# Kernel tuning notes

Hardware: AMD Instinct MI355X
Metric: run time of the kernel (lower is better)

The kernel has to match this reference:

```python
import jax, jax.numpy as jnp
import numpy as np

B, S, HID = 1, 2048, 2048
NH, NKV, HD = 16, 4, 128
G = NH // NKV  # queries per kv head (repeat_interleave factor)
QPA = 128      # query_pre_attn_scalar
EPS = 1e-6
SCALE = QPA ** -0.5
NEG = -1e9


def rms_norm(x, w, eps=EPS):
    return x * jax.lax.rsqrt(jnp.mean(x * x, axis=-1, keepdims=True) + eps) * w


def rope(x, cos, sin):
    # x: [B,S,H,D]; cos/sin: [S,D/2].
    # torch apply_rotary_emb: complex (x[:d/2] + i*x[d/2:]) * (cos + i*sin),
    # real parts -> first half, imag parts -> second half.
    d2 = x.shape[-1] // 2
    x1, x2 = x[..., :d2], x[..., d2:]
    c = cos[None, :, None, :]
    s = sin[None, :, None, :]
    return jnp.concatenate([x1 * c - x2 * s, x1 * s + x2 * c], axis=-1)


def setup_inputs() -> dict:
    key = jax.random.key(0)
    ks = jax.random.split(key, 4)
    hidden_states = jax.random.normal(ks[0], (B, S, HID), jnp.float32)
    inv_freq = 1.0 / (10000.0 ** (jnp.arange(0, HD, 2, dtype=jnp.float32) / HD))
    ang = jnp.arange(S, dtype=jnp.float32)[:, None] * inv_freq[None, :]  # [S, D/2]
    cos, sin = jnp.cos(ang), jnp.sin(ang)
    kv_write_indices = jnp.arange(S, dtype=jnp.int32)
    k_cache = jnp.zeros((B, S, NKV, HD), jnp.float32)
    v_cache = jnp.zeros((B, S, NKV, HD), jnp.float32)
    causal = jnp.tril(jnp.ones((S, S), dtype=bool))
    mask = jnp.where(causal, 0.0, NEG).astype(jnp.float32)[None, None]  # [1,1,S,S]
    qkv_out = (NH + 2 * NKV) * HD
    wqkv = jax.random.normal(ks[1], (qkv_out, HID), jnp.float32) * 0.02
    bqkv = jnp.zeros((qkv_out,), jnp.float32)
    wo = jax.random.normal(ks[2], (HID, NH * HD), jnp.float32) * 0.02
    bo = jnp.zeros((HID,), jnp.float32)
    q_norm_w = jnp.ones((HD,), jnp.float32)
    k_norm_w = jnp.ones((HD,), jnp.float32)
    return {"hidden_states": hidden_states, "cos": cos, "sin": sin,
            "k_cache": k_cache, "v_cache": v_cache, "mask": mask,
            "wqkv": wqkv, "bqkv": bqkv, "wo": wo, "bo": bo,
            "q_norm_w": q_norm_w, "k_norm_w": k_norm_w,
            "kv_write_indices": kv_write_indices}


def reference(hidden_states, cos, sin, k_cache, v_cache, mask,
              wqkv, bqkv, wo, bo, q_norm_w, k_norm_w, kv_write_indices):
    qkv = hidden_states @ wqkv.T + bqkv  # [B,S,(NH+2*NKV)*HD]
    q_sz, kv_sz = NH * HD, NKV * HD
    xq = qkv[..., :q_sz].reshape(B, S, NH, HD)
    xk = qkv[..., q_sz:q_sz + kv_sz].reshape(B, S, NKV, HD)
    xv = qkv[..., q_sz + kv_sz:].reshape(B, S, NKV, HD)
    xq = rope(rms_norm(xq, q_norm_w), cos, sin)
    xk = rope(rms_norm(xk, k_norm_w), cos, sin)
    k = k_cache.at[:, kv_write_indices].set(xk)  # index_copy_ on dim 1
    v = v_cache.at[:, kv_write_indices].set(xv)
    # GQA: head h attends with kv head h // G (repeat_interleave order)
    q = (xq * SCALE).reshape(B, S, NKV, G, HD)
    scores = jnp.einsum('bskgd,btkd->bkgst', q, k) + mask[:, :, None]  # [B,NKV,G,S,T]
    p = jax.nn.softmax(scores.astype(jnp.float32), axis=-1).astype(q.dtype)
    out = jnp.einsum('bkgst,btkd->bskgd', p, v).reshape(B, S, NH * HD)
    return out @ wo.T + bo
```

## Files before the change

kernel.cpp:

```cpp
#include <hip/hip_runtime.h>
#include <stdint.h>

#define S_LEN 2048
#define HIDN  2048
#define NH    16
#define NKV   4
#define HD    128
#define QKV_N 3072
#define Q_SZ  2048
#define SCALE_Q 0.12751743f

typedef __attribute__((ext_vector_type(8))) short  short8;
typedef __attribute__((ext_vector_type(4))) float  f32x4;

__device__ __forceinline__ uint16_t f2bf(float f) {
  uint32_t u = __float_as_uint(f);
  u += 0x7fffu + ((u >> 16) & 1u);
  return (uint16_t)(u >> 16);
}

__device__ __forceinline__ uint32_t cvtpk(float lo, float hi) {
  uint32_t r;
  asm("v_cvt_pk_bf16_f32 %0, %1, %2" : "=v"(r) : "v"(lo), "v"(hi));
  return r;
}

__device__ __forceinline__ void gload16(const void* g, void* lds_wave_base) {
  __builtin_amdgcn_global_load_lds(
      (const __attribute__((address_space(1))) uint32_t*)(uintptr_t)g,
      (__attribute__((address_space(3))) uint32_t*)(uint32_t)(uintptr_t)lds_wave_base,
      16, 0, 0);
}

__global__ __launch_bounds__(256) void cvt3_kernel(const float* __restrict__ a, uint16_t* __restrict__ oa, int na,
                                                   const float* __restrict__ b, uint16_t* __restrict__ ob, int nb,
                                                   const float* __restrict__ c, uint16_t* __restrict__ oc, int nc) {
  int i = (blockIdx.x * 256 + threadIdx.x) * 4;
  const float* src; uint16_t* dst; int j;
  if (i < na)           { src = a; dst = oa; j = i; }
  else if (i < na + nb) { src = b; dst = ob; j = i - na; }
  else if (i < na + nb + nc) { src = c; dst = oc; j = i - na - nb; }
  else return;
  float4 v = *(const float4*)(src + j);
  uint2 o;
  o.x = cvtpk(v.x, v.y);
  o.y = cvtpk(v.z, v.w);
  *(uint2*)(dst + j) = o;
}

#define BM 128
#define BN 128
#define BK 64
__global__ __launch_bounds__(512) void gemm_nt(const uint16_t* __restrict__ A,
                                               const uint16_t* __restrict__ B,
                                               const float* __restrict__ bias,
                                               float* __restrict__ C,
                                               int M, int N, int K) {
  __shared__ uint16_t As[2][BM * BK];
  __shared__ uint16_t Bs[2][BN * BK];
  const int tid = threadIdx.x;
  const int m0 = blockIdx.y * BM;
  const int n0 = blockIdx.x * BN;
  const int lane = tid & 63;
  const int w = tid >> 6;
  const int wm = (w >> 2) * 64, wn = (w & 3) * 32;
  const int lr = lane & 15, lg = lane >> 4;
  const int wb = w << 10;
  const int lb = wb + lane * 16;

  f32x4 acc[4][2];
#pragma unroll
  for (int i = 0; i < 4; ++i)
#pragma unroll
    for (int j = 0; j < 2; ++j) acc[i][j] = (f32x4){0.f, 0.f, 0.f, 0.f};

  auto stage = [&](int buf, int k0) {
#pragma unroll
    for (int i = 0; i < 2; ++i) {
      int bofs = i * 8192 + lb;
      int row = bofs >> 7;
      int colb = (bofs & 127) ^ ((row & 7) << 4);
      gload16((const char*)A + ((size_t)(m0 + row) * K + k0) * 2 + colb,
              (char*)As[buf] + i * 8192 + wb);
      gload16((const char*)B + ((size_t)(n0 + row) * K + k0) * 2 + colb,
              (char*)Bs[buf] + i * 8192 + wb);
    }
  };

  stage(0, 0);
  __syncthreads();
  const int nk = K / BK;
  for (int kk = 0; kk < nk; ++kk) {
    const int cur = kk & 1;
    if (kk + 1 < nk) stage(cur ^ 1, (kk + 1) * BK);
#pragma unroll
    for (int ks = 0; ks < 2; ++ks) {
      short8 av[4], bv[2];
#pragma unroll
      for (int i = 0; i < 4; ++i) {
        int row = wm + i * 16 + lr;
        av[i] = *(const short8*)((const char*)As[cur] + row * 128 + ((ks * 64 + lg * 16) ^ ((lr & 7) << 4)));
      }
#pragma unroll
      for (int j = 0; j < 2; ++j) {
        int row = wn + j * 16 + lr;
        bv[j] = *(const short8*)((const char*)Bs[cur] + row * 128 + ((ks * 64 + lg * 16) ^ ((lr & 7) << 4)));
      }
#pragma unroll
      for (int i = 0; i < 4; ++i)
#pragma unroll
        for (int j = 0; j < 2; ++j)
          acc[i][j] = __builtin_amdgcn_mfma_f32_16x16x32_bf16(av[i], bv[j], acc[i][j], 0, 0, 0);
    }
    __syncthreads();
  }
#pragma unroll
  for (int i = 0; i < 4; ++i) {
#pragma unroll
    for (int j = 0; j < 2; ++j) {
      int col = n0 + wn + j * 16 + lr;
      float bb = bias ? bias[col] : 0.f;
#pragma unroll
      for (int r = 0; r < 4; ++r) {
        int rowg = m0 + wm + i * 16 + lg * 4 + r;
        C[(size_t)rowg * N + col] = acc[i][j][r] + bb;
      }
    }
  }
}

#define QK_BLK (S_LEN * 20 / 4)
#define VT_BLK (NKV * (S_LEN / 64) * (HD / 64))
__global__ __launch_bounds__(256) void post_kernel(const float* __restrict__ qkv,
                                                   const float* __restrict__ cosb,
                                                   const float* __restrict__ sinb,
                                                   const float* __restrict__ qw,
                                                   const float* __restrict__ kw,
                                                   const int* __restrict__ widx,
                                                   uint16_t* __restrict__ Qo,
                                                   uint16_t* __restrict__ Ko,
                                                   uint16_t* __restrict__ Vt) {
  __shared__ float tile[64][68];
  int tid = threadIdx.x;
  if (blockIdx.x < QK_BLK) {
    int row = blockIdx.x * 4 + (tid >> 6);
    int lane = tid & 63;
    int t = row / 20, head = row % 20;
    bool isq = head < NH;
    int off = isq ? head * HD : Q_SZ + (head - NH) * HD;
    const float* x = qkv + (size_t)t * QKV_N + off;
    float x1 = x[lane], x2 = x[lane + 64];
    float ss = x1 * x1 + x2 * x2;
#pragma unroll
    for (int m = 1; m < 64; m <<= 1) ss += __shfl_xor(ss, m, 64);
    float rs = rsqrtf(ss * (1.0f / 128.0f) + 1e-6f);
    const float* wn_ = isq ? qw : kw;
    float n1 = x1 * rs * wn_[lane], n2 = x2 * rs * wn_[lane + 64];
    float c = cosb[t * 64 + lane], s = sinb[t * 64 + lane];
    float o1 = n1 * c - n2 * s;
    float o2 = n1 * s + n2 * c;
    if (isq) {
      o1 *= SCALE_Q; o2 *= SCALE_Q;
      uint16_t* dst = Qo + ((size_t)head * S_LEN + t) * HD;
      dst[lane] = f2bf(o1); dst[lane + 64] = f2bf(o2);
    } else {
      int td = widx[t];
      uint16_t* dst = Ko + ((size_t)(head - NH) * S_LEN + td) * HD;
      dst[lane] = f2bf(o1); dst[lane + 64] = f2bf(o2);
    }
  } else {
    int b = blockIdx.x - QK_BLK;
    int dt = b & 1;
    int tt = (b >> 1) & 31;
    int kh = b >> 6;
    int r = tid >> 2, c0 = tid & 3;
    const float* src = qkv + (size_t)(tt * 64 + r) * QKV_N + Q_SZ + NKV * HD + kh * HD + dt * 64;
#pragma unroll
    for (int i = 0; i < 4; ++i) {
      float4 v = *(const float4*)(src + (c0 + i * 4) * 4);
      *(float4*)&tile[r][(c0 + i * 4) * 4] = v;
    }
    __syncthreads();
    int rd = tid >> 2;
#pragma unroll
    for (int j = 0; j < 16; ++j) {
      int tloc = c0 * 16 + j;
      int tg = widx[tt * 64 + tloc];
      Vt[(size_t)(kh * HD + dt * 64 + rd) * S_LEN + tg] = f2bf(tile[tloc][rd]);
    }
  }
}

__global__ __launch_bounds__(256) void attn_kernel(const uint16_t* __restrict__ Q,
                                                   const uint16_t* __restrict__ Kc,
                                                   const uint16_t* __restrict__ Vt,
                                                   uint16_t* __restrict__ O) {
  __shared__ uint16_t Ks[2][64 * 128];
  __shared__ uint16_t Vs[2][128 * 64];
  __shared__ uint16_t Ps[4][16 * 64];

  const int x = blockIdx.x;
  const int half = x >> 8, rem = x & 255;
  const int h = rem >> 4, slot = rem & 15;
  const int qt = half ? slot : 31 - slot;
  const int kh = h >> 2;
  const int tid = threadIdx.x, w = tid >> 6, lane = tid & 63;
  const int lr = lane & 15, lg = lane >> 4;
  const int wb = w << 10, lb = wb + lane * 16;

  auto stage = [&](int buf, int t0) {
#pragma unroll
    for (int i = 0; i < 4; ++i) {
      int b = i * 4096 + lb;
      int rowK = b >> 8, colK = b & 255;
      gload16((const char*)Kc + ((size_t)kh * S_LEN + t0 + rowK) * (HD * 2) + (colK ^ ((rowK & 7) << 4)),
              (char*)Ks[buf] + i * 4096 + wb);
      int rowV = b >> 7, colV = b & 127;
      gload16((const char*)Vt + ((size_t)(kh * HD + rowV) * S_LEN + t0) * 2 + (colV ^ ((rowV & 7) << 4)),
              (char*)Vs[buf] + i * 4096 + wb);
    }
  };

  const int q0 = qt * 64;
  const int qw0 = q0 + w * 16;
  const int qg = qw0 + lr;

  short8 qf[4];
  const uint16_t* qb = Q + ((size_t)h * S_LEN + qw0 + lr) * HD;
#pragma unroll
  for (int ks = 0; ks < 4; ++ks) qf[ks] = *(const short8*)(qb + ks * 32 + lg * 8);

  f32x4 o[8];
#pragma unroll
  for (int d = 0; d < 8; ++d) o[d] = (f32x4){0.f, 0.f, 0.f, 0.f};
  float mrun = -1e30f, lrun = 0.f;

  const int ntiles = qt + 1;
  stage(0, 0);
  __syncthreads();

  for (int tt = 0; tt < ntiles; ++tt) {
    const int cur = tt & 1;
    const int t0 = tt * 64;
    if (tt + 1 < ntiles) stage(cur ^ 1, t0 + 64);

    f32x4 st[4];
    __builtin_amdgcn_s_setprio(1);
#pragma unroll
    for (int ts = 0; ts < 4; ++ts) {
      st[ts] = (f32x4){0.f, 0.f, 0.f, 0.f};
#pragma unroll
      for (int ks = 0; ks < 4; ++ks) {
        int row = ts * 16 + lr;
        int cb = (ks * 64 + lg * 16) ^ ((row & 7) << 4);
        short8 kf = *(const short8*)((const char*)Ks[cur] + row * 256 + cb);
        st[ts] = __builtin_amdgcn_mfma_f32_16x16x32_bf16(kf, qf[ks], st[ts], 0, 0, 0);
      }
    }
    __builtin_amdgcn_s_setprio(0);

    if (tt == ntiles - 1) {
#pragma unroll
      for (int ts = 0; ts < 4; ++ts)
#pragma unroll
        for (int r = 0; r < 4; ++r) {
          int tglob = t0 + ts * 16 + lg * 4 + r;
          if (tglob > qg) st[ts][r] = -1e9f;
        }
    }

    float pm = -1e30f;
#pragma unroll
    for (int ts = 0; ts < 4; ++ts)
#pragma unroll
      for (int r = 0; r < 4; ++r) pm = fmaxf(pm, st[ts][r]);
    pm = fmaxf(pm, __shfl_xor(pm, 16, 64));
    pm = fmaxf(pm, __shfl_xor(pm, 32, 64));

    const bool defer = __all(pm <= mrun + 8.0f) != 0;
    const float mnew = defer ? mrun : fmaxf(mrun, pm);

    float psum = 0.f;
#pragma unroll
    for (int ts = 0; ts < 4; ++ts)
#pragma unroll
      for (int r = 0; r < 4; ++r) {
        st[ts][r] = exp2f(st[ts][r] - mnew);
        psum += st[ts][r];
      }
    psum += __shfl_xor(psum, 16, 64);
    psum += __shfl_xor(psum, 32, 64);

    if (!defer) {
      float scl = exp2f(mrun - mnew);
      lrun *= scl;
      mrun = mnew;
#pragma unroll
      for (int r = 0; r < 4; ++r) {
        float s4 = __shfl(scl, (lane & 48) | (lg * 4 + r), 64);
#pragma unroll
        for (int d = 0; d < 8; ++d) o[d][r] *= s4;
      }
    }
    lrun += psum;

    {
      uint32_t* pw = (uint32_t*)&Ps[w][0];
#pragma unroll
      for (int ts = 0; ts < 4; ++ts)
#pragma unroll
        for (int rr = 0; rr < 2; ++rr)
          pw[lr * 32 + ((ts * 8 + lg * 2 + rr) ^ ((lr & 7) << 2))] =
              cvtpk(st[ts][2 * rr], st[ts][2 * rr + 1]);
    }

    __builtin_amdgcn_s_setprio(1);
#pragma unroll
    for (int ks = 0; ks < 2; ++ks) {
      short8 pf = *(const short8*)((const char*)&Ps[w][0] + lr * 128 + ((ks * 64 + lg * 16) ^ ((lr & 7) << 4)));
#pragma unroll
      for (int d = 0; d < 8; ++d) {
        int row = d * 16 + lr;
        int cb = (ks * 64 + lg * 16) ^ ((row & 7) << 4);
        short8 vf = *(const short8*)((const char*)Vs[cur] + row * 128 + cb);
        o[d] = __builtin_amdgcn_mfma_f32_16x16x32_bf16(pf, vf, o[d], 0, 0, 0);
      }
    }
    __builtin_amdgcn_s_setprio(0);

    __syncthreads();
  }

#pragma unroll
  for (int r = 0; r < 4; ++r) {
    float ls = __shfl(lrun, (lane & 48) | (lg * 4 + r), 64);
    float inv = 1.0f / ls;
    int qg2 = qw0 + lg * 4 + r;
    uint16_t* dst = O + ((size_t)qg2 * NH + h) * HD;
#pragma unroll
    for (int d = 0; d < 8; ++d) dst[d * 16 + lr] = f2bf(o[d][r] * inv);
  }
}

extern "C" void kernel_launch(void* const* d_in, const int* in_sizes, int n_in,
                              void* d_out, int out_size, void* d_ws, size_t ws_size,
                              hipStream_t stream) {
  const float* hidden = (const float*)d_in[0];
  const float* cosb   = (const float*)d_in[1];
  const float* sinb   = (const float*)d_in[2];
  const float* wqkv = (const float*)d_in[6];
  const float* bqkv = (const float*)d_in[7];
  const float* wo   = (const float*)d_in[8];
  const float* bo   = (const float*)d_in[9];
  const float* qnw  = (const float*)d_in[10];
  const float* knw  = (const float*)d_in[11];
  const int*   widx = (const int*)d_in[12];
  float* out = (float*)d_out;

  char* ws = (char*)d_ws;
  uint16_t* hb    = (uint16_t*)(ws);
  uint16_t* wqb   = (uint16_t*)(ws + (8u  << 20));
  uint16_t* wob   = (uint16_t*)(ws + (20u << 20));
  float*    qkv   = (float*)   (ws + (28u << 20));
  uint16_t* Qb    = (uint16_t*)(ws + (52u << 20));
  uint16_t* Kb    = (uint16_t*)(ws + (60u << 20));
  uint16_t* Vtb   = (uint16_t*)(ws + (62u << 20));
  uint16_t* attnb = (uint16_t*)(ws);

  const int na = S_LEN * HIDN, nb = QKV_N * HIDN, nc = HIDN * HIDN;
  cvt3_kernel<<<(na + nb + nc) / 4 / 256, 256, 0, stream>>>(hidden, hb, na, wqkv, wqb, nb, wo, wob, nc);

  gemm_nt<<<dim3(QKV_N / BN, S_LEN / BM), 512, 0, stream>>>(hb, wqb, bqkv, qkv,
                                                            S_LEN, QKV_N, HIDN);
  post_kernel<<<QK_BLK + VT_BLK, 256, 0, stream>>>(qkv, cosb, sinb, qnw, knw, widx, Qb, Kb, Vtb);
  attn_kernel<<<512, 256, 0, stream>>>(Qb, Kb, Vtb, attnb);
  gemm_nt<<<dim3(HIDN / BN, S_LEN / BM), 512, 0, stream>>>(attnb, wob, bo, out,
                                                           S_LEN, HIDN, HIDN);
}
```

Before: 255.2 us.

## Drop LDS K/V staging; read K/V fragments directly from global memory per wave

The attention kernel no longer double-buffers K and V tiles in shared memory with block-wide barriers. Each wave now reads its K and V MFMA fragments straight from global memory (relying on L1/L2 caching). The query-tile-to-wave mapping is also rebalanced so each wave owns an independent 16-row query chunk, pairing early and late chunks for causal load balance. This removes the LDS staging and syncthreads, but it gives up cross-wave reuse through LDS and exposes global-load latency directly in front of the MFMAs.

```diff
diff --git a/kernel.cpp b/kernel.cpp
--- a/kernel.cpp
+++ b/kernel.cpp
@@ -195,38 +195,23 @@
                                                    const uint16_t* __restrict__ Kc,
                                                    const uint16_t* __restrict__ Vt,
                                                    uint16_t* __restrict__ O) {
-  __shared__ uint16_t Ks[2][64 * 128];
-  __shared__ uint16_t Vs[2][128 * 64];
   __shared__ uint16_t Ps[4][16 * 64];
 
-  const int x = blockIdx.x;
-  const int half = x >> 8, rem = x & 255;
-  const int h = rem >> 4, slot = rem & 15;
-  const int qt = half ? slot : 31 - slot;
+  const int b = blockIdx.x;
+  const int h = b & 15, p = b >> 4;
   const int kh = h >> 2;
   const int tid = threadIdx.x, w = tid >> 6, lane = tid & 63;
   const int lr = lane & 15, lg = lane >> 4;
-  const int wb = w << 10, lb = wb + lane * 16;
-
-  auto stage = [&](int buf, int t0) {
-#pragma unroll
-    for (int i = 0; i < 4; ++i) {
-      int b = i * 4096 + lb;
-      int rowK = b >> 8, colK = b & 255;
-      gload16((const char*)Kc + ((size_t)kh * S_LEN + t0 + rowK) * (HD * 2) + (colK ^ ((rowK & 7) << 4)),
-              (char*)Ks[buf] + i * 4096 + wb);
-      int rowV = b >> 7, colV = b & 127;
-      gload16((const char*)Vt + ((size_t)(kh * HD + rowV) * S_LEN + t0) * 2 + (colV ^ ((rowV & 7) << 4)),
-              (char*)Vs[buf] + i * 4096 + wb);
-    }
-  };
-
-  const int q0 = qt * 64;
-  const int qw0 = q0 + w * 16;
-  const int qg = qw0 + lr;
+  const int c = ((w & 2) << 5) + ((w & 1) ? 63 - p : p);
+  const int q0 = c * 16;
+  const int qg = q0 + lr;
+  const int ntiles = c / 4 + 1;
+
+  const uint16_t* kbase = Kc + (size_t)kh * S_LEN * HD;
+  const uint16_t* vbase = Vt + (size_t)kh * HD * S_LEN;
 
   short8 qf[4];
-  const uint16_t* qb = Q + ((size_t)h * S_LEN + qw0 + lr) * HD;
+  const uint16_t* qb = Q + ((size_t)h * S_LEN + q0 + lr) * HD;
 #pragma unroll
   for (int ks = 0; ks < 4; ++ks) qf[ks] = *(const short8*)(qb + ks * 32 + lg * 8);
 
@@ -235,25 +220,18 @@
   for (int d = 0; d < 8; ++d) o[d] = (f32x4){0.f, 0.f, 0.f, 0.f};
   float mrun = -1e30f, lrun = 0.f;
 
-  const int ntiles = qt + 1;
-  stage(0, 0);
-  __syncthreads();
-
   for (int tt = 0; tt < ntiles; ++tt) {
-    const int cur = tt & 1;
     const int t0 = tt * 64;
-    if (tt + 1 < ntiles) stage(cur ^ 1, t0 + 64);
 
     f32x4 st[4];
     __builtin_amdgcn_s_setprio(1);
 #pragma unroll
     for (int ts = 0; ts < 4; ++ts) {
       st[ts] = (f32x4){0.f, 0.f, 0.f, 0.f};
+      const uint16_t* krow = kbase + (size_t)(t0 + ts * 16 + lr) * HD;
 #pragma unroll
       for (int ks = 0; ks < 4; ++ks) {
-        int row = ts * 16 + lr;
-        int cb = (ks * 64 + lg * 16) ^ ((row & 7) << 4);
-        short8 kf = *(const short8*)((const char*)Ks[cur] + row * 256 + cb);
+        short8 kf = *(const short8*)(krow + ks * 32 + lg * 8);
         st[ts] = __builtin_amdgcn_mfma_f32_16x16x32_bf16(kf, qf[ks], st[ts], 0, 0, 0);
       }
     }
@@ -314,28 +292,26 @@
               cvtpk(st[ts][2 * rr], st[ts][2 * rr + 1]);
     }
 
+    short8 pf0 = *(const short8*)((const char*)&Ps[w][0] + lr * 128 + ((lg * 16) ^ ((lr & 7) << 4)));
+    short8 pf1 = *(const short8*)((const char*)&Ps[w][0] + lr * 128 + ((64 + lg * 16) ^ ((lr & 7) << 4)));
+
     __builtin_amdgcn_s_setprio(1);
 #pragma unroll
-    for (int ks = 0; ks < 2; ++ks) {
-      short8 pf = *(const short8*)((const char*)&Ps[w][0] + lr * 128 + ((ks * 64 + lg * 16) ^ ((lr & 7) << 4)));
-#pragma unroll
-      for (int d = 0; d < 8; ++d) {
-        int row = d * 16 + lr;
-        int cb = (ks * 64 + lg * 16) ^ ((row & 7) << 4);
-        short8 vf = *(const short8*)((const char*)Vs[cur] + row * 128 + cb);
-        o[d] = __builtin_amdgcn_mfma_f32_16x16x32_bf16(pf, vf, o[d], 0, 0, 0);
-      }
+    for (int d = 0; d < 8; ++d) {
+      const uint16_t* vrow = vbase + (size_t)(d * 16 + lr) * S_LEN + t0;
+      short8 vf0 = *(const short8*)(vrow + lg * 8);
+      short8 vf1 = *(const short8*)(vrow + 32 + lg * 8);
+      o[d] = __builtin_amdgcn_mfma_f32_16x16x32_bf16(pf0, vf0, o[d], 0, 0, 0);
+      o[d] = __builtin_amdgcn_mfma_f32_16x16x32_bf16(pf1, vf1, o[d], 0, 0, 0);
     }
     __builtin_amdgcn_s_setprio(0);
-
-    __syncthreads();
   }
 
 #pragma unroll
   for (int r = 0; r < 4; ++r) {
     float ls = __shfl(lrun, (lane & 48) | (lg * 4 + r), 64);
     float inv = 1.0f / ls;
-    int qg2 = qw0 + lg * 4 + r;
+    int qg2 = q0 + lg * 4 + r;
     uint16_t* dst = O + ((size_t)qg2 * NH + h) * HD;
 #pragma unroll
     for (int d = 0; d < 8; ++d) dst[d * 16 + lr] = f2bf(o[d][r] * inv);
```

Measured after the change: 374.1 us. +46.6%, slower.
